# Optimization experiments

Hardware: AMD Instinct MI355X
Metric: run time of the kernel (lower is better)

Reference implementation:

```python
import jax, jax.numpy as jnp
import numpy as np

D_MODEL = 1024
NUM_HEADS = 16
DEPTH = D_MODEL // NUM_HEADS
EPS = 1e-6


def setup_inputs() -> dict:
    key = jax.random.key(0)
    ks = jax.random.split(key, 9)
    B, S = 4, 2048
    scale = 1.0 / np.sqrt(D_MODEL)
    inp = {
        "inputs": jax.random.normal(ks[0], (B, S, D_MODEL), dtype=jnp.float32),
        "Wq": jax.random.normal(ks[1], (D_MODEL, D_MODEL), dtype=jnp.float32) * scale,
        "bq": jnp.zeros((D_MODEL,), dtype=jnp.float32),
        "Wk": jax.random.normal(ks[2], (D_MODEL, D_MODEL), dtype=jnp.float32) * scale,
        "bk": jnp.zeros((D_MODEL,), dtype=jnp.float32),
        "Wv": jax.random.normal(ks[3], (D_MODEL, D_MODEL), dtype=jnp.float32) * scale,
        "bv": jnp.zeros((D_MODEL,), dtype=jnp.float32),
        "Wo": jax.random.normal(ks[4], (D_MODEL, D_MODEL), dtype=jnp.float32) * scale,
        "bo": jnp.zeros((D_MODEL,), dtype=jnp.float32),
        "gamma": jnp.ones((D_MODEL,), dtype=jnp.float32),
        "beta": jnp.zeros((D_MODEL,), dtype=jnp.float32),
    }
    return inp


def _layer_norm(x, gamma, beta):
    mu = jnp.mean(x, axis=-1, keepdims=True)
    var = jnp.mean(jnp.square(x - mu), axis=-1, keepdims=True)
    return (x - mu) * jax.lax.rsqrt(var + EPS) * gamma + beta


def reference(inputs, Wq, bq, Wk, bk, Wv, bv, Wo, bo, gamma, beta):
    B, S, _ = inputs.shape
    # QKV projections, split heads: [B, H, S, depth]
    def split_heads(x):
        return x.reshape(B, S, NUM_HEADS, DEPTH).transpose(0, 2, 1, 3)

    q = split_heads(inputs @ Wq + bq)
    k = split_heads(inputs @ Wk + bk)
    v = split_heads(inputs @ Wv + bv)

    # scores: [B, H, S, S]
    scores = jnp.einsum("bhqd,bhkd->bhqk", q, k) / jnp.sqrt(
        jnp.asarray(DEPTH, dtype=inputs.dtype))
    attn = jax.nn.softmax(scores, axis=-1)  # dropout is identity in eval mode
    out = jnp.einsum("bhqk,bhkd->bhqd", attn, v)
    out = out.transpose(0, 2, 1, 3).reshape(B, S, D_MODEL)
    out = out @ Wo + bo  # dropout2 identity in eval mode
    return _layer_norm(inputs + out, gamma, beta)
```

## Files before the change

### kernel.cpp

```cpp
#include <hip/hip_runtime.h>
#include <hip/hip_bf16.h>


typedef __bf16 bf16;
typedef __bf16 bf16x4 __attribute__((ext_vector_type(4)));
typedef __bf16 bf16x8 __attribute__((ext_vector_type(8)));
typedef float floatx4 __attribute__((ext_vector_type(4)));

#define MFMA16(a, b, c) __builtin_amdgcn_mfma_f32_16x16x32_bf16((a), (b), (c), 0, 0, 0)

static __device__ __forceinline__ floatx4 vmax4(floatx4 a, floatx4 b) {
    floatx4 r;
    r[0] = fmaxf(a[0], b[0]); r[1] = fmaxf(a[1], b[1]);
    r[2] = fmaxf(a[2], b[2]); r[3] = fmaxf(a[3], b[3]);
    return r;
}

__global__ __launch_bounds__(256) void convert_kernel(
    const float* __restrict__ x, bf16* __restrict__ xb)
{
    const int i = blockIdx.x * 256 + threadIdx.x;
    const float4 v = ((const float4*)x)[i];
    bf16x4 r;
    r[0] = (bf16)v.x; r[1] = (bf16)v.y; r[2] = (bf16)v.z; r[3] = (bf16)v.w;
    ((bf16x4*)xb)[i] = r;
}

__global__ __launch_bounds__(256) void transpose_kernel(
    const float* __restrict__ Wq, const float* __restrict__ Wk,
    const float* __restrict__ Wv, const float* __restrict__ Wo,
    bf16* __restrict__ WT, bf16* __restrict__ WoT)
{
    __shared__ float tile[32][33];
    const int z = blockIdx.z;
    const float* src = (z == 0) ? Wq : (z == 1) ? Wk : (z == 2) ? Wv : Wo;
    bf16* dst = (z < 3) ? (WT + (long)z * 1024 * 1024) : WoT;
    const int n0 = blockIdx.x * 32, k0 = blockIdx.y * 32;
    const int tx = threadIdx.x & 31, ty = threadIdx.x >> 5;
#pragma unroll
    for (int i = 0; i < 32; i += 8)
        tile[ty + i][tx] = src[(long)(k0 + ty + i) * 1024 + n0 + tx];
    __syncthreads();
#pragma unroll
    for (int i = 0; i < 32; i += 8)
        dst[(long)(n0 + ty + i) * 1024 + k0 + tx] = (bf16)tile[tx][ty + i];
}

template <int MODE>
__global__ __launch_bounds__(256, 2) void gemm_kernel(
    const bf16* __restrict__ A, const bf16* __restrict__ Bt,
    const float* __restrict__ b0, const float* __restrict__ b1,
    const float* __restrict__ b2, const float* __restrict__ X,
    bf16* __restrict__ Qo, bf16* __restrict__ Ko, bf16* __restrict__ Vto,
    float* __restrict__ Tmp, int N, int K)
{
    constexpr int LDT = 40;
    __shared__ __align__(16) bf16 As[128 * LDT];
    __shared__ __align__(16) bf16 Bs[128 * LDT];
    const int t = threadIdx.x;
    const int lane = t & 63;
    const int w = t >> 6;
    const int wm = w >> 1, wn = w & 1;
    const int g = lane >> 4, c = lane & 15;
    const int bm = blockIdx.y * 128;
    const int bn = blockIdx.x * 128;

    const int srow = t >> 2;
    const int scol = (t & 3) * 8;

    floatx4 acc[4][4];
#pragma unroll
    for (int i = 0; i < 4; ++i)
#pragma unroll
        for (int j = 0; j < 4; ++j) acc[i][j] = floatx4{0.f, 0.f, 0.f, 0.f};

    const bf16* Ap0 = A + (long)(bm + srow) * K + scol;
    const bf16* Ap1 = A + (long)(bm + 64 + srow) * K + scol;
    const bf16* Bp0 = Bt + (long)(bn + srow) * K + scol;
    const bf16* Bp1 = Bt + (long)(bn + 64 + srow) * K + scol;

    uint4 a0 = *(const uint4*)(Ap0);
    uint4 a1 = *(const uint4*)(Ap1);
    uint4 q0 = *(const uint4*)(Bp0);
    uint4 q1 = *(const uint4*)(Bp1);

    for (int k0 = 0; k0 < K; k0 += 32) {
        __syncthreads();
        *(uint4*)&As[srow * LDT + scol] = a0;
        *(uint4*)&As[(64 + srow) * LDT + scol] = a1;
        *(uint4*)&Bs[srow * LDT + scol] = q0;
        *(uint4*)&Bs[(64 + srow) * LDT + scol] = q1;
        __syncthreads();
        if (k0 + 32 < K) {
            a0 = *(const uint4*)(Ap0 + k0 + 32);
            a1 = *(const uint4*)(Ap1 + k0 + 32);
            q0 = *(const uint4*)(Bp0 + k0 + 32);
            q1 = *(const uint4*)(Bp1 + k0 + 32);
        }
        bf16x8 af[4], bfv[4];
#pragma unroll
        for (int i = 0; i < 4; ++i)
            af[i] = *(const bf16x8*)&As[(wm * 64 + i * 16 + c) * LDT + g * 8];
#pragma unroll
        for (int j = 0; j < 4; ++j)
            bfv[j] = *(const bf16x8*)&Bs[(wn * 64 + j * 16 + c) * LDT + g * 8];
#pragma unroll
        for (int i = 0; i < 4; ++i)
#pragma unroll
            for (int j = 0; j < 4; ++j)
                acc[i][j] = MFMA16(af[i], bfv[j], acc[i][j]);
    }

    if (MODE == 0) {
#pragma unroll
        for (int j = 0; j < 4; ++j) {
            const int col = bn + wn * 64 + j * 16 + c;
            const int sec = col >> 10;
            const int nn = col & 1023;
            const int h = nn >> 6, dd = nn & 63;
            const float* bp = (sec == 0) ? b0 : (sec == 1) ? b1 : b2;
            const float bias = bp[nn];
#pragma unroll
            for (int i = 0; i < 4; ++i) {
                const int r0 = bm + wm * 64 + i * 16 + g * 4;
                if (sec == 2) {
                    bf16x4 pack;
#pragma unroll
                    for (int reg = 0; reg < 4; ++reg)
                        pack[reg] = (bf16)(acc[i][j][reg] + bias);
                    const int b_ = r0 >> 11, sr = r0 & 2047;
                    *(bf16x4*)&Vto[((long)(b_ * 16 + h) * 64 + dd) * 2048 + sr] = pack;
                } else {
#pragma unroll
                    for (int reg = 0; reg < 4; ++reg) {
                        const int r = r0 + reg;
                        const int b_ = r >> 11, sr = r & 2047;
                        const float v = acc[i][j][reg] + bias;
                        if (sec == 0)
                            Qo[((long)(b_ * 16 + h) * 2048 + sr) * 64 + dd] =
                                (bf16)(v * 0.18033688011112042f);
                        else
                            Ko[((long)(b_ * 16 + h) * 2048 + sr) * 64 + dd] = (bf16)v;
                    }
                }
            }
        }
    } else {
#pragma unroll
        for (int j = 0; j < 4; ++j) {
            const int col = bn + wn * 64 + j * 16 + c;
            const float bias = b0[col];
#pragma unroll
            for (int i = 0; i < 4; ++i) {
#pragma unroll
                for (int reg = 0; reg < 4; ++reg) {
                    const int r = bm + wm * 64 + i * 16 + g * 4 + reg;
                    Tmp[(long)r * N + col] =
                        acc[i][j][reg] + bias + X[(long)r * N + col];
                }
            }
        }
    }
}

__global__ __launch_bounds__(256, 2) void flash_kernel(
    const bf16* __restrict__ Q, const bf16* __restrict__ Kc,
    const bf16* __restrict__ Vt, bf16* __restrict__ O)
{
    constexpr int KSTR = 72;
    constexpr int VSTR = 136;
    constexpr int PSTR = 136;
    __shared__ __align__(16) bf16 Ks[128 * KSTR];
    __shared__ __align__(16) bf16 Vs[64 * VSTR];
    __shared__ __align__(16) bf16 Pl[4 * 16 * PSTR];
    const int t = threadIdx.x;
    const int lane = t & 63;
    const int w = t >> 6;
    const int g = lane >> 4, c = lane & 15;
    const int bh = blockIdx.x;
    const int b_ = bh >> 4, h = bh & 15;
    const bf16* Qp = Q + (long)bh * 2048 * 64;
    const bf16* Kp = Kc + (long)bh * 2048 * 64;
    const bf16* Vp = Vt + (long)bh * 64 * 2048;
    const int q0 = blockIdx.y * 128 + w * 32;
    bf16* Pw = Pl + w * 16 * PSTR;

    bf16x8 qf[2][2];
#pragma unroll
    for (int qs = 0; qs < 2; ++qs)
#pragma unroll
        for (int p = 0; p < 2; ++p)
            qf[qs][p] = *(const bf16x8*)(Qp + (long)(q0 + qs * 16 + c) * 64 + p * 32 + g * 8);

    float m_c[2] = {-1e30f, -1e30f};
    float l_c[2] = {0.f, 0.f};
    floatx4 o[2][4];
#pragma unroll
    for (int qs = 0; qs < 2; ++qs)
#pragma unroll
        for (int dd = 0; dd < 4; ++dd) o[qs][dd] = floatx4{0.f, 0.f, 0.f, 0.f};

    for (int kt = 0; kt < 16; ++kt) {
        __syncthreads();
        {
            uint4 kr[4], vr[4];
#pragma unroll
            for (int i = 0; i < 4; ++i) {
                const int idx = i * 256 + t;
                kr[i] = *(const uint4*)(Kp + (long)kt * 8192 + idx * 8);
                const int vd = idx >> 4, vsc = idx & 15;
                vr[i] = *(const uint4*)(Vp + (long)vd * 2048 + kt * 128 + vsc * 8);
            }
#pragma unroll
            for (int i = 0; i < 4; ++i) {
                const int idx = i * 256 + t;
                *(uint4*)&Ks[(idx >> 3) * KSTR + (idx & 7) * 8] = kr[i];
                *(uint4*)&Vs[(idx >> 4) * VSTR + (idx & 15) * 8] = vr[i];
            }
        }
        __syncthreads();

#pragma unroll
        for (int qs = 0; qs < 2; ++qs) {
            floatx4 s[8];
#pragma unroll
            for (int ks = 0; ks < 8; ++ks) {
                bf16x8 kf0 = *(const bf16x8*)&Ks[(ks * 16 + c) * KSTR + g * 8];
                bf16x8 kf1 = *(const bf16x8*)&Ks[(ks * 16 + c) * KSTR + 32 + g * 8];
                floatx4 z = floatx4{0.f, 0.f, 0.f, 0.f};
                z = MFMA16(kf0, qf[qs][0], z);
                z = MFMA16(kf1, qf[qs][1], z);
                s[ks] = z;
            }
            floatx4 t0 = vmax4(s[0], s[1]);
            floatx4 t1 = vmax4(s[2], s[3]);
            floatx4 t2 = vmax4(s[4], s[5]);
            floatx4 t3 = vmax4(s[6], s[7]);
            t0 = vmax4(vmax4(t0, t1), vmax4(t2, t3));
            float mx = fmaxf(fmaxf(t0[0], t0[1]), fmaxf(t0[2], t0[3]));
            mx = fmaxf(mx, __shfl_xor(mx, 16, 64));
            mx = fmaxf(mx, __shfl_xor(mx, 32, 64));
            const float mn = fmaxf(m_c[qs], mx);
            const float al = __builtin_amdgcn_exp2f(m_c[qs] - mn);
            m_c[qs] = mn;
            floatx4 a4 = floatx4{0.f, 0.f, 0.f, 0.f};
#pragma unroll
            for (int ks = 0; ks < 8; ++ks) {
#pragma unroll
                for (int r = 0; r < 4; ++r)
                    s[ks][r] = __builtin_amdgcn_exp2f(s[ks][r] - mn);
                a4 += s[ks];
            }
            float rs = (a4[0] + a4[1]) + (a4[2] + a4[3]);
            rs += __shfl_xor(rs, 16, 64);
            rs += __shfl_xor(rs, 32, 64);
            l_c[qs] = l_c[qs] * al + rs;
            float al_r[4];
#pragma unroll
            for (int r = 0; r < 4; ++r) al_r[r] = __shfl(al, g * 4 + r, 64);
#pragma unroll
            for (int dd = 0; dd < 4; ++dd)
#pragma unroll
                for (int r = 0; r < 4; ++r) o[qs][dd][r] *= al_r[r];
#pragma unroll
            for (int ks = 0; ks < 8; ++ks) {
                bf16x4 pk;
#pragma unroll
                for (int r = 0; r < 4; ++r) pk[r] = (bf16)s[ks][r];
                *(bf16x4*)&Pw[c * PSTR + ks * 16 + g * 4] = pk;
            }
            asm volatile("s_waitcnt lgkmcnt(0)" ::: "memory");
#pragma unroll
            for (int kk = 0; kk < 4; ++kk) {
                bf16x8 pf = *(const bf16x8*)&Pw[c * PSTR + kk * 32 + g * 8];
#pragma unroll
                for (int dd = 0; dd < 4; ++dd) {
                    bf16x8 vf = *(const bf16x8*)&Vs[(dd * 16 + c) * VSTR + kk * 32 + g * 8];
                    o[qs][dd] = MFMA16(pf, vf, o[qs][dd]);
                }
            }
        }
    }

#pragma unroll
    for (int qs = 0; qs < 2; ++qs) {
        float linv[4];
#pragma unroll
        for (int r = 0; r < 4; ++r) linv[r] = 1.0f / __shfl(l_c[qs], g * 4 + r, 64);
#pragma unroll
        for (int dd = 0; dd < 4; ++dd)
#pragma unroll
            for (int r = 0; r < 4; ++r) {
                const float v = o[qs][dd][r] * linv[r];
                const int q = q0 + qs * 16 + g * 4 + r;
                O[((long)b_ * 2048 + q) * 1024 + h * 64 + dd * 16 + c] = (bf16)v;
            }
    }
}

__global__ __launch_bounds__(256, 2) void ln_kernel(
    const float* __restrict__ Tmp, const float* __restrict__ gamma,
    const float* __restrict__ beta, float* __restrict__ out)
{
    const int row = blockIdx.x;
    const int t = threadIdx.x;
    const int lane = t & 63, w = t >> 6;
    const float4 v = ((const float4*)(Tmp + (long)row * 1024))[t];
    float s = v.x + v.y + v.z + v.w;
    float ss = v.x * v.x + v.y * v.y + v.z * v.z + v.w * v.w;
#pragma unroll
    for (int off = 1; off < 64; off <<= 1) {
        s += __shfl_xor(s, off, 64);
        ss += __shfl_xor(ss, off, 64);
    }
    __shared__ float sb[4], ssb[4];
    if (lane == 0) { sb[w] = s; ssb[w] = ss; }
    __syncthreads();
    s = sb[0] + sb[1] + sb[2] + sb[3];
    ss = ssb[0] + ssb[1] + ssb[2] + ssb[3];
    const float mu = s * (1.0f / 1024.0f);
    const float var = ss * (1.0f / 1024.0f) - mu * mu;
    const float inv = rsqrtf(var + 1e-6f);
    const float4 gm = ((const float4*)gamma)[t];
    const float4 bt = ((const float4*)beta)[t];
    float4 r;
    r.x = (v.x - mu) * inv * gm.x + bt.x;
    r.y = (v.y - mu) * inv * gm.y + bt.y;
    r.z = (v.z - mu) * inv * gm.z + bt.z;
    r.w = (v.w - mu) * inv * gm.w + bt.w;
    ((float4*)(out + (long)row * 1024))[t] = r;
}

extern "C" void kernel_launch(void* const* d_in, const int* in_sizes, int n_in,
                              void* d_out, int out_size, void* d_ws, size_t ws_size,
                              hipStream_t stream)
{
    const float* x     = (const float*)d_in[0];
    const float* Wq    = (const float*)d_in[1];
    const float* bq    = (const float*)d_in[2];
    const float* Wk    = (const float*)d_in[3];
    const float* bk    = (const float*)d_in[4];
    const float* Wv    = (const float*)d_in[5];
    const float* bv    = (const float*)d_in[6];
    const float* Wo    = (const float*)d_in[7];
    const float* bo    = (const float*)d_in[8];
    const float* gamma = (const float*)d_in[9];
    const float* beta  = (const float*)d_in[10];
    float* out = (float*)d_out;

    char* ws = (char*)d_ws;
    bf16* xb   = (bf16*)(ws);
    bf16* WT   = (bf16*)(ws + 16777216);
    bf16* Qb   = (bf16*)(ws + 23068672);
    bf16* Kb   = (bf16*)(ws + 39845888);
    bf16* WoT  = (bf16*)(ws + 56623104);
    float* Tmp = (float*)(ws);
    bf16* Vtb  = (bf16*)d_out;
    bf16* Ob   = (bf16*)((char*)d_out + 16777216);

    convert_kernel<<<8192, 256, 0, stream>>>(x, xb);
    transpose_kernel<<<dim3(32, 32, 4), 256, 0, stream>>>(Wq, Wk, Wv, Wo, WT, WoT);
    gemm_kernel<0><<<dim3(24, 64), 256, 0, stream>>>(
        xb, WT, bq, bk, bv, nullptr, Qb, Kb, Vtb, nullptr, 3072, 1024);
    flash_kernel<<<dim3(64, 16), 256, 0, stream>>>(Qb, Kb, Vtb, Ob);
    gemm_kernel<1><<<dim3(8, 64), 256, 0, stream>>>(
        Ob, WoT, bo, nullptr, nullptr, x, nullptr, nullptr, nullptr, Tmp, 1024, 1024);
    ln_kernel<<<8192, 256, 0, stream>>>(Tmp, gamma, beta, out);
}
```

Measured before the change: 354.0 us.

## Interleave both query subtiles in flash loop and store residual sum in bf16

```diff
diff --git a/kernel.cpp b/kernel.cpp
--- a/kernel.cpp
+++ b/kernel.cpp
@@ -52,7 +52,7 @@
     const float* __restrict__ b0, const float* __restrict__ b1,
     const float* __restrict__ b2, const float* __restrict__ X,
     bf16* __restrict__ Qo, bf16* __restrict__ Ko, bf16* __restrict__ Vto,
-    float* __restrict__ Tmp, int N, int K)
+    bf16* __restrict__ Tmpb, int N, int K)
 {
     constexpr int LDT = 40;
     __shared__ __align__(16) bf16 As[128 * LDT];
@@ -155,8 +155,8 @@
 #pragma unroll
                 for (int reg = 0; reg < 4; ++reg) {
                     const int r = bm + wm * 64 + i * 16 + g * 4 + reg;
-                    Tmp[(long)r * N + col] =
-                        acc[i][j][reg] + bias + X[(long)r * N + col];
+                    Tmpb[(long)r * N + col] =
+                        (bf16)(acc[i][j][reg] + bias + X[(long)r * N + col]);
                 }
             }
         }
@@ -172,7 +172,7 @@
     constexpr int PSTR = 136;
     __shared__ __align__(16) bf16 Ks[128 * KSTR];
     __shared__ __align__(16) bf16 Vs[64 * VSTR];
-    __shared__ __align__(16) bf16 Pl[4 * 16 * PSTR];
+    __shared__ __align__(16) bf16 Pl[4 * 32 * PSTR];
     const int t = threadIdx.x;
     const int lane = t & 63;
     const int w = t >> 6;
@@ -183,7 +183,7 @@
     const bf16* Kp = Kc + (long)bh * 2048 * 64;
     const bf16* Vp = Vt + (long)bh * 64 * 2048;
     const int q0 = blockIdx.y * 128 + w * 32;
-    bf16* Pw = Pl + w * 16 * PSTR;
+    bf16* Pw = Pl + w * 32 * PSTR;
 
     bf16x8 qf[2][2];
 #pragma unroll
@@ -220,22 +220,26 @@
         }
         __syncthreads();
 
-#pragma unroll
-        for (int qs = 0; qs < 2; ++qs) {
-            floatx4 s[8];
-#pragma unroll
-            for (int ks = 0; ks < 8; ++ks) {
-                bf16x8 kf0 = *(const bf16x8*)&Ks[(ks * 16 + c) * KSTR + g * 8];
-                bf16x8 kf1 = *(const bf16x8*)&Ks[(ks * 16 + c) * KSTR + 32 + g * 8];
+        floatx4 s[2][8];
+#pragma unroll
+        for (int ks = 0; ks < 8; ++ks) {
+            bf16x8 kf0 = *(const bf16x8*)&Ks[(ks * 16 + c) * KSTR + g * 8];
+            bf16x8 kf1 = *(const bf16x8*)&Ks[(ks * 16 + c) * KSTR + 32 + g * 8];
+#pragma unroll
+            for (int qs = 0; qs < 2; ++qs) {
                 floatx4 z = floatx4{0.f, 0.f, 0.f, 0.f};
                 z = MFMA16(kf0, qf[qs][0], z);
                 z = MFMA16(kf1, qf[qs][1], z);
-                s[ks] = z;
-            }
-            floatx4 t0 = vmax4(s[0], s[1]);
-            floatx4 t1 = vmax4(s[2], s[3]);
-            floatx4 t2 = vmax4(s[4], s[5]);
-            floatx4 t3 = vmax4(s[6], s[7]);
+                s[qs][ks] = z;
+            }
+        }
+
+#pragma unroll
+        for (int qs = 0; qs < 2; ++qs) {
+            floatx4 t0 = vmax4(s[qs][0], s[qs][1]);
+            floatx4 t1 = vmax4(s[qs][2], s[qs][3]);
+            floatx4 t2 = vmax4(s[qs][4], s[qs][5]);
+            floatx4 t3 = vmax4(s[qs][6], s[qs][7]);
             t0 = vmax4(vmax4(t0, t1), vmax4(t2, t3));
             float mx = fmaxf(fmaxf(t0[0], t0[1]), fmaxf(t0[2], t0[3]));
             mx = fmaxf(mx, __shfl_xor(mx, 16, 64));
@@ -248,8 +252,8 @@
             for (int ks = 0; ks < 8; ++ks) {
 #pragma unroll
                 for (int r = 0; r < 4; ++r)
-                    s[ks][r] = __builtin_amdgcn_exp2f(s[ks][r] - mn);
-                a4 += s[ks];
+                    s[qs][ks][r] = __builtin_amdgcn_exp2f(s[qs][ks][r] - mn);
+                a4 += s[qs][ks];
             }
             float rs = (a4[0] + a4[1]) + (a4[2] + a4[3]);
             rs += __shfl_xor(rs, 16, 64);
@@ -266,18 +270,20 @@
             for (int ks = 0; ks < 8; ++ks) {
                 bf16x4 pk;
 #pragma unroll
-                for (int r = 0; r < 4; ++r) pk[r] = (bf16)s[ks][r];
-                *(bf16x4*)&Pw[c * PSTR + ks * 16 + g * 4] = pk;
-            }
-            asm volatile("s_waitcnt lgkmcnt(0)" ::: "memory");
-#pragma unroll
-            for (int kk = 0; kk < 4; ++kk) {
-                bf16x8 pf = *(const bf16x8*)&Pw[c * PSTR + kk * 32 + g * 8];
-#pragma unroll
-                for (int dd = 0; dd < 4; ++dd) {
-                    bf16x8 vf = *(const bf16x8*)&Vs[(dd * 16 + c) * VSTR + kk * 32 + g * 8];
-                    o[qs][dd] = MFMA16(pf, vf, o[qs][dd]);
-                }
+                for (int r = 0; r < 4; ++r) pk[r] = (bf16)s[qs][ks][r];
+                *(bf16x4*)&Pw[(qs * 16 + c) * PSTR + ks * 16 + g * 4] = pk;
+            }
+        }
+        asm volatile("s_waitcnt lgkmcnt(0)" ::: "memory");
+#pragma unroll
+        for (int kk = 0; kk < 4; ++kk) {
+            bf16x8 pf0 = *(const bf16x8*)&Pw[(0 + c) * PSTR + kk * 32 + g * 8];
+            bf16x8 pf1 = *(const bf16x8*)&Pw[(16 + c) * PSTR + kk * 32 + g * 8];
+#pragma unroll
+            for (int dd = 0; dd < 4; ++dd) {
+                bf16x8 vf = *(const bf16x8*)&Vs[(dd * 16 + c) * VSTR + kk * 32 + g * 8];
+                o[0][dd] = MFMA16(pf0, vf, o[0][dd]);
+                o[1][dd] = MFMA16(pf1, vf, o[1][dd]);
             }
         }
     }
@@ -299,15 +305,16 @@
 }
 
 __global__ __launch_bounds__(256, 2) void ln_kernel(
-    const float* __restrict__ Tmp, const float* __restrict__ gamma,
+    const bf16* __restrict__ Tmp, const float* __restrict__ gamma,
     const float* __restrict__ beta, float* __restrict__ out)
 {
     const int row = blockIdx.x;
     const int t = threadIdx.x;
     const int lane = t & 63, w = t >> 6;
-    const float4 v = ((const float4*)(Tmp + (long)row * 1024))[t];
-    float s = v.x + v.y + v.z + v.w;
-    float ss = v.x * v.x + v.y * v.y + v.z * v.z + v.w * v.w;
+    const bf16x4 vb = ((const bf16x4*)(Tmp + (long)row * 1024))[t];
+    const float xv[4] = {(float)vb[0], (float)vb[1], (float)vb[2], (float)vb[3]};
+    float s = xv[0] + xv[1] + xv[2] + xv[3];
+    float ss = xv[0] * xv[0] + xv[1] * xv[1] + xv[2] * xv[2] + xv[3] * xv[3];
 #pragma unroll
     for (int off = 1; off < 64; off <<= 1) {
         s += __shfl_xor(s, off, 64);
@@ -324,10 +331,10 @@
     const float4 gm = ((const float4*)gamma)[t];
     const float4 bt = ((const float4*)beta)[t];
     float4 r;
-    r.x = (v.x - mu) * inv * gm.x + bt.x;
-    r.y = (v.y - mu) * inv * gm.y + bt.y;
-    r.z = (v.z - mu) * inv * gm.z + bt.z;
-    r.w = (v.w - mu) * inv * gm.w + bt.w;
+    r.x = (xv[0] - mu) * inv * gm.x + bt.x;
+    r.y = (xv[1] - mu) * inv * gm.y + bt.y;
+    r.z = (xv[2] - mu) * inv * gm.z + bt.z;
+    r.w = (xv[3] - mu) * inv * gm.w + bt.w;
     ((float4*)(out + (long)row * 1024))[t] = r;
 }
 
@@ -354,7 +361,7 @@
     bf16* Qb   = (bf16*)(ws + 23068672);
     bf16* Kb   = (bf16*)(ws + 39845888);
     bf16* WoT  = (bf16*)(ws + 56623104);
-    float* Tmp = (float*)(ws);
+    bf16* Tmpb = (bf16*)(ws);
     bf16* Vtb  = (bf16*)d_out;
     bf16* Ob   = (bf16*)((char*)d_out + 16777216);
 
@@ -364,6 +371,6 @@
         xb, WT, bq, bk, bv, nullptr, Qb, Kb, Vtb, nullptr, 3072, 1024);
     flash_kernel<<<dim3(64, 16), 256, 0, stream>>>(Qb, Kb, Vtb, Ob);
     gemm_kernel<1><<<dim3(8, 64), 256, 0, stream>>>(
-        Ob, WoT, bo, nullptr, nullptr, x, nullptr, nullptr, nullptr, Tmp, 1024, 1024);
-    ln_kernel<<<8192, 256, 0, stream>>>(Tmp, gamma, beta, out);
-}
+        Ob, WoT, bo, nullptr, nullptr, x, nullptr, nullptr, nullptr, Tmpb, 1024, 1024);
+    ln_kernel<<<8192, 256, 0, stream>>>(Tmpb, gamma, beta, out);
+}
```

Result: faster. 343.8 us (-2.9%).
